# Kernel tuning notes

Hardware: AMD Instinct MI355X
Metric: run time of the kernel (lower is better)

## Reference

```python
import jax, jax.numpy as jnp
import numpy as np

B, H, W, C = 8, 128, 128, 128


def setup_inputs() -> dict:
    key = jax.random.key(0)
    ks = jax.random.split(key, 6)
    shape = (B, H, W, C)
    inp = {f"t{i+1}": jax.random.normal(ks[i], shape, dtype=jnp.float32) for i in range(5)}
    # One (1,1,5,1) kernel per channel, 'uniform' init in keras -> U[-0.05, 0.05].
    inp["w"] = jax.random.uniform(ks[5], (5, C), dtype=jnp.float32, minval=-0.05, maxval=0.05)
    return inp


def reference(t1, t2, t3, t4, t5, w):
    # Per-channel 1x1 conv over the 5 stacked streams is exactly a per-channel
    # weighted sum: out[b,h,w,c] = sum_j w[j,c] * t_j[b,h,w,c].
    return (t1 * w[0] + t2 * w[1] + t3 * w[2] + t4 * w[3] + t5 * w[4])
```

## Files before the change

### kernel.cpp

```cpp
#include <hip/hip_runtime.h>


typedef float fvec4 __attribute__((ext_vector_type(4)));

#define NPER 4
#define BLOCKS 4096
#define THREADS 256
#define STRIDE (BLOCKS * THREADS)

__global__ __launch_bounds__(THREADS) void merge5_kernel(
    const float* __restrict__ t1, const float* __restrict__ t2,
    const float* __restrict__ t3, const float* __restrict__ t4,
    const float* __restrict__ t5, const float* __restrict__ w,
    float* __restrict__ out)
{
    const int tid = blockIdx.x * THREADS + threadIdx.x;

    const int c4 = (tid & 31) << 2;
    const fvec4 w0 = *(const fvec4*)(w + 0 * 128 + c4);
    const fvec4 w1 = *(const fvec4*)(w + 1 * 128 + c4);
    const fvec4 w2 = *(const fvec4*)(w + 2 * 128 + c4);
    const fvec4 w3 = *(const fvec4*)(w + 3 * 128 + c4);
    const fvec4 w4 = *(const fvec4*)(w + 4 * 128 + c4);

    fvec4 a[NPER], b[NPER], c[NPER], d[NPER], e[NPER];

#pragma unroll
    for (int i = 0; i < NPER; ++i) {
        const int idx = tid + i * STRIDE;
        a[i] = ((const fvec4*)t1)[idx];
        b[i] = ((const fvec4*)t2)[idx];
        c[i] = ((const fvec4*)t3)[idx];
        d[i] = ((const fvec4*)t4)[idx];
        e[i] = ((const fvec4*)t5)[idx];
    }

#pragma unroll
    for (int i = 0; i < NPER; ++i) {
        fvec4 r = a[i] * w0 + b[i] * w1 + c[i] * w2 + d[i] * w3 + e[i] * w4;
        const int idx = tid + i * STRIDE;
        __builtin_nontemporal_store(r, (fvec4*)out + idx);
    }
}

extern "C" void kernel_launch(void* const* d_in, const int* in_sizes, int n_in,
                              void* d_out, int out_size, void* d_ws, size_t ws_size,
                              hipStream_t stream) {
    const float* t1 = (const float*)d_in[0];
    const float* t2 = (const float*)d_in[1];
    const float* t3 = (const float*)d_in[2];
    const float* t4 = (const float*)d_in[3];
    const float* t5 = (const float*)d_in[4];
    const float* w  = (const float*)d_in[5];
    float* out = (float*)d_out;

    merge5_kernel<<<BLOCKS, THREADS, 0, stream>>>(t1, t2, t3, t4, t5, w, out);
}
```

Baseline: 315.6 us.

## Software-pipeline loads with one-ahead prefetch over fewer, longer-running blocks

Halves the grid to 2048 blocks, each processing 8 strided chunks instead of 4. Instead of issuing all loads up front, it double-buffers: it loads the next iteration's five vectors while computing and storing the current one. It also switches from nontemporal stores to regular stores. Fewer loads are in flight per thread, which may limit memory-level parallelism for this bandwidth-bound kernel. The regular stores may also pollute the cache.

```diff
diff --git a/kernel.cpp b/kernel.cpp
--- a/kernel.cpp
+++ b/kernel.cpp
@@ -3,10 +3,10 @@
 
 typedef float fvec4 __attribute__((ext_vector_type(4)));
 
-#define NPER 4
-#define BLOCKS 4096
 #define THREADS 256
-#define STRIDE (BLOCKS * THREADS)
+#define BLOCKS  2048
+#define NITER   8
+#define STRIDE  (BLOCKS * THREADS)
 
 __global__ __launch_bounds__(THREADS) void merge5_kernel(
     const float* __restrict__ t1, const float* __restrict__ t2,
@@ -23,23 +23,27 @@
     const fvec4 w3 = *(const fvec4*)(w + 3 * 128 + c4);
     const fvec4 w4 = *(const fvec4*)(w + 4 * 128 + c4);
 
-    fvec4 a[NPER], b[NPER], c[NPER], d[NPER], e[NPER];
+    fvec4 a0 = ((const fvec4*)t1)[tid];
+    fvec4 b0 = ((const fvec4*)t2)[tid];
+    fvec4 c0 = ((const fvec4*)t3)[tid];
+    fvec4 d0 = ((const fvec4*)t4)[tid];
+    fvec4 e0 = ((const fvec4*)t5)[tid];
 
 #pragma unroll
-    for (int i = 0; i < NPER; ++i) {
-        const int idx = tid + i * STRIDE;
-        a[i] = ((const fvec4*)t1)[idx];
-        b[i] = ((const fvec4*)t2)[idx];
-        c[i] = ((const fvec4*)t3)[idx];
-        d[i] = ((const fvec4*)t4)[idx];
-        e[i] = ((const fvec4*)t5)[idx];
-    }
-
-#pragma unroll
-    for (int i = 0; i < NPER; ++i) {
-        fvec4 r = a[i] * w0 + b[i] * w1 + c[i] * w2 + d[i] * w3 + e[i] * w4;
-        const int idx = tid + i * STRIDE;
-        __builtin_nontemporal_store(r, (fvec4*)out + idx);
+    for (int i = 0; i < NITER; ++i) {
+        const int idx  = tid + i * STRIDE;
+        fvec4 a1, b1, c1, d1, e1;
+        if (i + 1 < NITER) {
+            const int nidx = idx + STRIDE;
+            a1 = ((const fvec4*)t1)[nidx];
+            b1 = ((const fvec4*)t2)[nidx];
+            c1 = ((const fvec4*)t3)[nidx];
+            d1 = ((const fvec4*)t4)[nidx];
+            e1 = ((const fvec4*)t5)[nidx];
+        }
+        fvec4 r = a0 * w0 + b0 * w1 + c0 * w2 + d0 * w3 + e0 * w4;
+        ((fvec4*)out)[idx] = r;
+        a0 = a1; b0 = b1; c0 = c1; d0 = d1; e0 = e1;
     }
 }
 
```

After: 307.6 us. -2.5%, faster.
